# Optimization experiments

Measured on AMD Instinct MI355X. Metric: run time of the kernel, lower is better.

Reference implementation:

```python
import jax, jax.numpy as jnp
import numpy as np

B, L = 16384, 1024
BIAS = (1, 1)


def setup_inputs() -> dict:
    key = jax.random.key(0)
    k1, k2 = jax.random.split(key)
    c = jax.random.normal(k1, (B, L), dtype=jnp.float32)
    y = jax.random.randint(k2, (B, L), 0, 2, dtype=jnp.int32)
    return {"c": c, "y": y}


def reference(c, y):
    # BPMLL loss. The double sum over (k,l) in Y_i x Ybar_i of exp(c_l - c_k)
    # factors exactly: (sum_k y_k exp(-c_k)) * (sum_l ybar_l exp(c_l)).
    y_f = y.astype(jnp.float32)          # [B, L]
    y_bar = 1.0 - y_f                    # [B, L]
    y_norm = jnp.sum(y_f, axis=1) ** BIAS[0]        # [B]
    y_bar_norm = jnp.sum(y_bar, axis=1) ** BIAS[1]  # [B]
    pos_term = jnp.sum(y_f * jnp.exp(-c), axis=1)   # sum_k y_k exp(-c_k)
    neg_term = jnp.sum(y_bar * jnp.exp(c), axis=1)  # sum_l ybar_l exp(c_l)
    loss = (pos_term * neg_term) / (y_norm * y_bar_norm)  # [B]
    return jnp.mean(loss)  # reduction='mean' -> scalar
```

## Files before the change

### kernel.cpp

```cpp
#include <hip/hip_runtime.h>


#define NROWS 16384
#define NCOLS 1024
#define WPB 4
#define NBLOCKS 512
#define ROWS_PER_WAVE (NROWS / (NBLOCKS * WPB))

typedef float vf4 __attribute__((ext_vector_type(4)));
typedef int vi4 __attribute__((ext_vector_type(4)));

__device__ __forceinline__ void elem(float cv, int yv,
                                     float& pos, float& neg, float& cnt) {
    float t = __expf(yv ? -cv : cv);
    pos += yv ? t : 0.f;
    neg += yv ? 0.f : t;
    cnt += (float)yv;
}

__device__ __forceinline__ void consume4(const vf4& cv, const vi4& yv,
                                         float& pos, float& neg, float& cnt) {
    elem(cv.x, yv.x, pos, neg, cnt);
    elem(cv.y, yv.y, pos, neg, cnt);
    elem(cv.z, yv.z, pos, neg, cnt);
    elem(cv.w, yv.w, pos, neg, cnt);
}

__device__ __forceinline__ float row_finish(float pos, float neg, float cnt) {
#pragma unroll
    for (int off = 1; off < 64; off <<= 1) {
        pos += __shfl_xor(pos, off);
        neg += __shfl_xor(neg, off);
        cnt += __shfl_xor(cnt, off);
    }
    return (pos * neg) / (cnt * ((float)NCOLS - cnt));
}

__global__ __launch_bounds__(256, 2) void bpmll_rows_kernel(
    const float* __restrict__ c, const int* __restrict__ y,
    float* __restrict__ partials) {
    const int wave = threadIdx.x >> 6;
    const int lane = threadIdx.x & 63;
    const int gw = blockIdx.x * WPB + wave;
    const int row0 = gw * ROWS_PER_WAVE;

    const vf4* __restrict__ cp = (const vf4*)(c + (size_t)row0 * NCOLS);
    const vi4* __restrict__ yp = (const vi4*)(y + (size_t)row0 * NCOLS);

    vf4 cbuf[2][4];
    vi4 ybuf[2][4];

#pragma unroll
    for (int i = 0; i < 4; ++i)
        cbuf[0][i] = __builtin_nontemporal_load(&cp[lane + 64 * i]);
#pragma unroll
    for (int i = 0; i < 4; ++i)
        ybuf[0][i] = __builtin_nontemporal_load(&yp[lane + 64 * i]);

    float wave_loss = 0.f;
#pragma unroll
    for (int r = 0; r < ROWS_PER_WAVE; ++r) {
        const int cur = r & 1, nxt = cur ^ 1;
        if (r < ROWS_PER_WAVE - 1) {
            const vf4* cn = cp + (size_t)(r + 1) * (NCOLS / 4);
            const vi4* yn = yp + (size_t)(r + 1) * (NCOLS / 4);
#pragma unroll
            for (int i = 0; i < 4; ++i)
                cbuf[nxt][i] = __builtin_nontemporal_load(&cn[lane + 64 * i]);
#pragma unroll
            for (int i = 0; i < 4; ++i)
                ybuf[nxt][i] = __builtin_nontemporal_load(&yn[lane + 64 * i]);
        }
        float pos = 0.f, neg = 0.f, cnt = 0.f;
#pragma unroll
        for (int i = 0; i < 4; ++i)
            consume4(cbuf[cur][i], ybuf[cur][i], pos, neg, cnt);
        wave_loss += row_finish(pos, neg, cnt);
    }

    __shared__ float acc[WPB];
    if (lane == 0) acc[wave] = wave_loss;
    __syncthreads();
    if (threadIdx.x == 0) {
        partials[blockIdx.x] =
            (acc[0] + acc[1] + acc[2] + acc[3]) * (1.0f / (float)NROWS);
    }
}

__global__ __launch_bounds__(256) void bpmll_reduce_kernel(
    const float* __restrict__ partials, float* __restrict__ out) {
    float s = partials[threadIdx.x] + partials[threadIdx.x + 256];
#pragma unroll
    for (int off = 1; off < 64; off <<= 1) s += __shfl_xor(s, off);

    __shared__ float smem[4];
    const int lane = threadIdx.x & 63;
    const int wave = threadIdx.x >> 6;
    if (lane == 0) smem[wave] = s;
    __syncthreads();
    if (threadIdx.x == 0) out[0] = smem[0] + smem[1] + smem[2] + smem[3];
}

extern "C" void kernel_launch(void* const* d_in, const int* in_sizes, int n_in,
                              void* d_out, int out_size, void* d_ws, size_t ws_size,
                              hipStream_t stream) {
    const float* c = (const float*)d_in[0];
    const int* y = (const int*)d_in[1];
    float* partials = (float*)d_ws;
    float* out = (float*)d_out;

    bpmll_rows_kernel<<<NBLOCKS, 256, 0, stream>>>(c, y, partials);
    bpmll_reduce_kernel<<<1, 256, 0, stream>>>(partials, out);
}
```

Before: 137.4 us.

## Use one row per wave with inline-asm streaming loads and many blocks

Replaces the persistent multi-row-per-wave double-buffered loop with one row per wave and 4096 blocks. All eight 16-byte loads are issued up front through inline-asm global_load_dwordx4 with sc0 sc1 nt bits, followed by a single waitcnt. Occupancy hints rise to 6 blocks per CU so memory latency is hidden by parallelism rather than software prefetch. The reduce kernel now sums 4096 partials instead of 512. The inline asm ties the code to this ISA's cache-bit syntax, and dropping the loop removes in-wave overlap between loading and computing.

```diff
diff --git a/kernel.cpp b/kernel.cpp
--- a/kernel.cpp
+++ b/kernel.cpp
@@ -4,8 +4,7 @@
 #define NROWS 16384
 #define NCOLS 1024
 #define WPB 4
-#define NBLOCKS 512
-#define ROWS_PER_WAVE (NROWS / (NBLOCKS * WPB))
+#define NBLOCKS (NROWS / WPB)
 
 typedef float vf4 __attribute__((ext_vector_type(4)));
 typedef int vi4 __attribute__((ext_vector_type(4)));
@@ -26,60 +25,50 @@
     elem(cv.w, yv.w, pos, neg, cnt);
 }
 
-__device__ __forceinline__ float row_finish(float pos, float neg, float cnt) {
+#define STREAM_LD(dst, addr, off_str)                                  \
+    asm volatile("global_load_dwordx4 %0, %1, off" off_str " sc0 sc1 nt" \
+                 : "=v"(dst) : "v"(addr))
+
+__global__ __launch_bounds__(256, 6) void bpmll_rows_kernel(
+    const float* __restrict__ c, const int* __restrict__ y,
+    float* __restrict__ partials) {
+    const int wave = threadIdx.x >> 6;
+    const int lane = threadIdx.x & 63;
+    const int row = blockIdx.x * WPB + wave;
+
+    const char* cp = (const char*)(c + (size_t)row * NCOLS) + lane * 16;
+    const char* yp = (const char*)(y + (size_t)row * NCOLS) + lane * 16;
+
+    vf4 cb0, cb1, cb2, cb3;
+    vi4 yb0, yb1, yb2, yb3;
+    STREAM_LD(cb0, cp, "");
+    STREAM_LD(cb1, cp, " offset:1024");
+    STREAM_LD(cb2, cp, " offset:2048");
+    STREAM_LD(cb3, cp, " offset:3072");
+    STREAM_LD(yb0, yp, "");
+    STREAM_LD(yb1, yp, " offset:1024");
+    STREAM_LD(yb2, yp, " offset:2048");
+    STREAM_LD(yb3, yp, " offset:3072");
+
+    asm volatile("s_waitcnt vmcnt(0)" ::: "memory");
+    __builtin_amdgcn_sched_barrier(0);
+
+    float pos = 0.f, neg = 0.f, cnt = 0.f;
+    consume4(cb0, yb0, pos, neg, cnt);
+    consume4(cb1, yb1, pos, neg, cnt);
+    consume4(cb2, yb2, pos, neg, cnt);
+    consume4(cb3, yb3, pos, neg, cnt);
+
 #pragma unroll
     for (int off = 1; off < 64; off <<= 1) {
         pos += __shfl_xor(pos, off);
         neg += __shfl_xor(neg, off);
         cnt += __shfl_xor(cnt, off);
     }
-    return (pos * neg) / (cnt * ((float)NCOLS - cnt));
-}
-
-__global__ __launch_bounds__(256, 2) void bpmll_rows_kernel(
-    const float* __restrict__ c, const int* __restrict__ y,
-    float* __restrict__ partials) {
-    const int wave = threadIdx.x >> 6;
-    const int lane = threadIdx.x & 63;
-    const int gw = blockIdx.x * WPB + wave;
-    const int row0 = gw * ROWS_PER_WAVE;
-
-    const vf4* __restrict__ cp = (const vf4*)(c + (size_t)row0 * NCOLS);
-    const vi4* __restrict__ yp = (const vi4*)(y + (size_t)row0 * NCOLS);
-
-    vf4 cbuf[2][4];
-    vi4 ybuf[2][4];
-
-#pragma unroll
-    for (int i = 0; i < 4; ++i)
-        cbuf[0][i] = __builtin_nontemporal_load(&cp[lane + 64 * i]);
-#pragma unroll
-    for (int i = 0; i < 4; ++i)
-        ybuf[0][i] = __builtin_nontemporal_load(&yp[lane + 64 * i]);
-
-    float wave_loss = 0.f;
-#pragma unroll
-    for (int r = 0; r < ROWS_PER_WAVE; ++r) {
-        const int cur = r & 1, nxt = cur ^ 1;
-        if (r < ROWS_PER_WAVE - 1) {
-            const vf4* cn = cp + (size_t)(r + 1) * (NCOLS / 4);
-            const vi4* yn = yp + (size_t)(r + 1) * (NCOLS / 4);
-#pragma unroll
-            for (int i = 0; i < 4; ++i)
-                cbuf[nxt][i] = __builtin_nontemporal_load(&cn[lane + 64 * i]);
-#pragma unroll
-            for (int i = 0; i < 4; ++i)
-                ybuf[nxt][i] = __builtin_nontemporal_load(&yn[lane + 64 * i]);
-        }
-        float pos = 0.f, neg = 0.f, cnt = 0.f;
-#pragma unroll
-        for (int i = 0; i < 4; ++i)
-            consume4(cbuf[cur][i], ybuf[cur][i], pos, neg, cnt);
-        wave_loss += row_finish(pos, neg, cnt);
-    }
+    const float loss = (pos * neg) / (cnt * ((float)NCOLS - cnt));
 
     __shared__ float acc[WPB];
-    if (lane == 0) acc[wave] = wave_loss;
+    if (lane == 0) acc[wave] = loss;
     __syncthreads();
     if (threadIdx.x == 0) {
         partials[blockIdx.x] =
@@ -89,7 +78,9 @@
 
 __global__ __launch_bounds__(256) void bpmll_reduce_kernel(
     const float* __restrict__ partials, float* __restrict__ out) {
-    float s = partials[threadIdx.x] + partials[threadIdx.x + 256];
+    float s = 0.f;
+#pragma unroll
+    for (int i = 0; i < 16; ++i) s += partials[threadIdx.x + 256 * i];
 #pragma unroll
     for (int off = 1; off < 64; off <<= 1) s += __shfl_xor(s, off);
 
```

Result: no change. 138.2 us (+0.6%).
